# Kernel optimization log

Hardware: AMD Instinct MI355X
Metric: run time of the kernel (lower is better)

The kernel has to match this reference:

```python
import jax, jax.numpy as jnp
import numpy as np

COMMITMENT_COST = 0.25
EPS = 1e-10


def setup_inputs() -> dict:
    key = jax.random.key(0)
    k1, k2 = jax.random.split(key)
    B, C, H, W = 16, 64, 128, 128          # C == embedding_dim
    K, D = 512, 64                          # codebook size, embedding_dim
    inputs = jax.random.normal(k1, (B, C, H, W), dtype=jnp.float32)
    # nn.Embedding init: uniform(-1/K, 1/K)
    embedding = jax.random.uniform(k2, (K, D), dtype=jnp.float32,
                                   minval=-1.0 / K, maxval=1.0 / K)
    return {"inputs": inputs, "embedding": embedding}


def reference(inputs, embedding):
    # NCHW -> NHWC, flatten to tokens [N, D]
    x = jnp.transpose(inputs, (0, 2, 3, 1))
    nhwc_shape = x.shape
    flat = x.reshape(-1, embedding.shape[1])                       # [N, D]

    distances = (jnp.sum(flat * flat, axis=1, keepdims=True)
                 + jnp.sum(embedding * embedding, axis=1)
                 - 2.0 * flat @ embedding.T)
    idx = jnp.argmin(distances, axis=1)                            # [N]

    # one-hot encodings (returned), quantized via direct gather
    encodings = jax.nn.one_hot(idx, embedding.shape[0], dtype=flat.dtype)  # [N, K]
    quantized = embedding[idx].reshape(nhwc_shape)                 # [B,H,W,D]

    e_latent = jnp.mean((jax.lax.stop_gradient(quantized) - x) ** 2)
    q_latent = jnp.mean((quantized - jax.lax.stop_gradient(x)) ** 2)
    loss = q_latent + COMMITMENT_COST * e_latent

    # straight-through estimator
    quantized_st = x + jax.lax.stop_gradient(quantized - x)

    avg_probs = jnp.mean(encodings, axis=0)                        # [K]
    perplexity = jnp.exp(-jnp.sum(avg_probs * jnp.log(avg_probs + EPS)))

    return (loss, jnp.transpose(quantized_st, (0, 3, 1, 2)), perplexity, encodings)
```

## Files before the change

### kernel.cpp

```cpp
#include <hip/hip_runtime.h>
#include <math.h>


#define NTOK    262144
#define KCODES  512
#define DDIM    64
#define CSTRIDE 16384
#define IMG     1048576
#define QOFF    1
#define POFF    16777217
#define EOFF    16777218
#define BK      8192
#define LOSS    8704
#define EBF     12800
#define SUBFLT  32768

typedef short bf16x8 __attribute__((ext_vector_type(8)));
typedef float f32x4  __attribute__((ext_vector_type(4)));

__device__ __forceinline__ unsigned short f2bf(float f) {
    unsigned u = __float_as_uint(f);
    return (unsigned short)((u + 0x7fffu + ((u >> 16) & 1u)) >> 16);
}

__device__ __forceinline__ float np_pairwise_sq64(const float* v) {
    float r[8];
#pragma unroll
    for (int j = 0; j < 8; ++j) r[j] = __fmul_rn(v[j], v[j]);
#pragma unroll
    for (int i = 8; i < 64; i += 8) {
#pragma unroll
        for (int j = 0; j < 8; ++j)
            r[j] = __fadd_rn(r[j], __fmul_rn(v[i + j], v[i + j]));
    }
    float s01 = __fadd_rn(r[0], r[1]);
    float s23 = __fadd_rn(r[2], r[3]);
    float s45 = __fadd_rn(r[4], r[5]);
    float s67 = __fadd_rn(r[6], r[7]);
    return __fadd_rn(__fadd_rn(s01, s23), __fadd_rn(s45, s67));
}

__global__ __launch_bounds__(256) void vq_prep(const float* __restrict__ emb,
                                               float* __restrict__ out,
                                               float* __restrict__ ws) {
    const int tid = threadIdx.x, blk = blockIdx.x;
    if (blk >= 9) {
        f32x4* sub4 = (f32x4*)(out + EOFF) + (size_t)(blk - 9) * 8192;
        const f32x4 z4 = {0.f, 0.f, 0.f, 0.f};
#pragma unroll
        for (int ii = 0; ii < 32; ++ii)
            sub4[ii * 256 + tid] = z4;
        return;
    }
    if (blk < 8) {
        unsigned short* ebf = (unsigned short*)(ws + EBF);
#pragma unroll
        for (int ii = 0; ii < 16; ++ii) {
            int t = blk * 4096 + ii * 256 + tid;
            ebf[t] = f2bf(emb[t]);
        }
    } else {
#pragma unroll
        for (int r = 0; r < 2; ++r) {
            const int k = tid * 2 + r;
            const float* e = emb + (size_t)k * DDIM;
            float v[64];
#pragma unroll
            for (int i = 0; i < 64; ++i) v[i] = e[i];
            ws[BK + k] = np_pairwise_sq64(v);
        }
    }
}

__global__ __launch_bounds__(256, 4) void vq_main(const float* __restrict__ in,
                                                  const float* __restrict__ emb,
                                                  float* __restrict__ out,
                                                  float* __restrict__ ws) {
    __shared__ unsigned short xbf[64 * 68];
    __shared__ float          xls[64 * 64];
    __shared__ float          bsh[512];
    __shared__ int            idx_sh[64];
    __shared__ float          red[4];

    const int tid = threadIdx.x, blk = blockIdx.x;
    const int T0 = blk * 64, b = T0 >> 14, hw0 = T0 & 16383;

    const float4* gx = (const float4*)(in + (size_t)b * IMG + hw0);
    float4 g[4];
#pragma unroll
    for (int jj = 0; jj < 4; ++jj) {
        int t = tid + jj * 256;
        g[jj] = gx[(size_t)(t >> 4) * (CSTRIDE / 4) + (t & 15)];
    }
    const float bk0 = ws[BK + tid];
    const float bk1 = ws[BK + 256 + tid];

#pragma unroll
    for (int jj = 0; jj < 4; ++jj) {
        int t = tid + jj * 256;
        int c = t >> 4, q4 = (t & 15) * 4;
        *(float4*)(&xls[c * 64 + q4]) = g[jj];
        xbf[(q4 + 0) * 68 + c] = f2bf(g[jj].x);
        xbf[(q4 + 1) * 68 + c] = f2bf(g[jj].y);
        xbf[(q4 + 2) * 68 + c] = f2bf(g[jj].z);
        xbf[(q4 + 3) * 68 + c] = f2bf(g[jj].w);
    }
    bsh[tid]       = bk0;
    bsh[256 + tid] = bk1;
    __syncthreads();

    const int l = tid & 63, w = tid >> 6;
    const int lm = l & 15, lg = l >> 4;

    const bf16x8 a0 = *(const bf16x8*)(xbf + (w * 16 + lm) * 68 + lg * 8);
    const bf16x8 a1 = *(const bf16x8*)(xbf + (w * 16 + lm) * 68 + 32 + lg * 8);

    const unsigned short* ebf = (const unsigned short*)(ws + EBF);
    const unsigned short* ep  = ebf + lm * 64 + lg * 8;

    float dmin[4]; int idx[4];
#pragma unroll
    for (int r = 0; r < 4; ++r) { dmin[r] = 3.402823466e38f; idx[r] = 0; }
    const f32x4 zero = {0.f, 0.f, 0.f, 0.f};

#pragma unroll 4
    for (int nt = 0; nt < 32; ++nt) {
        bf16x8 b0 = *(const bf16x8*)(ep + nt * 1024);
        bf16x8 b1 = *(const bf16x8*)(ep + nt * 1024 + 32);
        f32x4 acc = __builtin_amdgcn_mfma_f32_16x16x32_bf16(a0, b0, zero, 0, 0, 0);
        acc       = __builtin_amdgcn_mfma_f32_16x16x32_bf16(a1, b1, acc,  0, 0, 0);
        const int   code = nt * 16 + lm;
        const float bk   = bsh[code];
#pragma unroll
        for (int r = 0; r < 4; ++r) {
            float s = fmaf(-2.0f, acc[r], bk);
            if (s < dmin[r]) { dmin[r] = s; idx[r] = code; }
        }
    }

#pragma unroll
    for (int m = 1; m < 16; m <<= 1) {
#pragma unroll
        for (int r = 0; r < 4; ++r) {
            float od = __shfl_xor(dmin[r], m, 64);
            int   oi = __shfl_xor(idx[r],  m, 64);
            if (od < dmin[r] || (od == dmin[r] && oi < idx[r])) {
                dmin[r] = od; idx[r] = oi;
            }
        }
    }
    if (lm == 0) {
#pragma unroll
        for (int r = 0; r < 4; ++r) idx_sh[w * 16 + lg * 4 + r] = idx[r];
    }
    __syncthreads();

    const int tl = tid & 63, chh = (tid >> 6) * 16;
    const int id = idx_sh[tl];

    const float4* e4 = (const float4*)(emb + (size_t)id * DDIM + chh);
    float4 ev[4];
#pragma unroll
    for (int k = 0; k < 4; ++k) ev[k] = e4[k];

    float* q = out + QOFF + (size_t)b * IMG + hw0 + tl;
    float lsum = 0.f;
#pragma unroll
    for (int cc = 0; cc < 16; ++cc) {
        float x   = xls[(chh + cc) * 64 + tl];
        float ee  = ((const float*)&ev[cc >> 2])[cc & 3];
        float dqx = __fsub_rn(ee, x);
        lsum = __fadd_rn(lsum, __fmul_rn(dqx, dqx));
        __builtin_nontemporal_store(__fadd_rn(x, dqx),
                                    q + (size_t)(chh + cc) * CSTRIDE);
    }
#pragma unroll
    for (int off = 32; off > 0; off >>= 1) lsum += __shfl_down(lsum, off, 64);
    if ((tid & 63) == 0) red[tid >> 6] = lsum;
    __syncthreads();
    if (tid == 0) ws[LOSS + blk] = red[0] + red[1] + red[2] + red[3];

    if (tid < 64) {
        const int ix = idx_sh[tid];
        __builtin_nontemporal_store(
            1.0f, out + EOFF + (size_t)blk * SUBFLT + tid * 512 + ix);
        atomicAdd((int*)ws + ((blk & 15) << 9) + ix, 1);
    }
}

__global__ void vq_final(float* __restrict__ out, const float* __restrict__ ws) {
    __shared__ float sl[512], sp[512];
    int t = threadIdx.x;
    float s = 0.f;
#pragma unroll
    for (int r = 0; r < 8; ++r) s += ws[LOSS + t + 512 * r];
    sl[t] = s;
    int cnt = 0;
#pragma unroll
    for (int r = 0; r < 16; ++r) cnt += ((const int*)ws)[(r << 9) + t];
    float p = (float)cnt * (1.0f / 262144.0f);
    sp[t] = p * logf(p + 1e-10f);
    __syncthreads();
    for (int off = 256; off > 0; off >>= 1) {
        if (t < off) { sl[t] += sl[t + off]; sp[t] += sp[t + off]; }
        __syncthreads();
    }
    if (t == 0) {
        float m = sl[0] * (1.0f / 16777216.0f);
        out[0]    = __fadd_rn(m, __fmul_rn(0.25f, m));
        out[POFF] = expf(-sp[0]);
    }
}

extern "C" void kernel_launch(void* const* d_in, const int* in_sizes, int n_in,
                              void* d_out, int out_size, void* d_ws, size_t ws_size,
                              hipStream_t stream) {
    const float* in  = (const float*)d_in[0];
    const float* emb = (const float*)d_in[1];
    float* out = (float*)d_out;
    float* ws  = (float*)d_ws;

    (void)hipMemsetAsync(d_ws, 0, 16 * 512 * sizeof(int), stream);
    hipLaunchKernelGGL(vq_prep,  dim3(4105), dim3(256), 0, stream, emb, out, ws);
    hipLaunchKernelGGL(vq_main,  dim3(4096), dim3(256), 0, stream, in, emb, out, ws);
    hipLaunchKernelGGL(vq_final, dim3(1),    dim3(512), 0, stream, out, ws);
}
```

Baseline: 740.1 us.

## Move one-hot zeroing into main kernel and split quantized write into separate pass

The zero-fill of the one-hot encodings moves from the prep kernel into vq_main, so each block clears its own 64x512 slice with nontemporal vector stores, and the slice base is offset by two floats to keep the vector stores aligned. The quantized/loss write is taken out of vq_main into a new vq_qwrite kernel. It reads the input again together with a uint16 index array stored in workspace, and gathers embedding values per channel in a coalesced pattern. This drops the big xls shared buffer from vq_main, which may help occupancy. In exchange the 64 MB input is read a second time and one more kernel launch is added.

After: 754.4 us. About the same (+1.9%).

```diff
diff --git a/kernel.cpp b/kernel.cpp
--- a/kernel.cpp
+++ b/kernel.cpp
@@ -13,10 +13,12 @@
 #define BK      8192
 #define LOSS    8704
 #define EBF     12800
+#define IDXOFF  29184
 #define SUBFLT  32768
 
 typedef short bf16x8 __attribute__((ext_vector_type(8)));
 typedef float f32x4  __attribute__((ext_vector_type(4)));
+typedef float f32x2  __attribute__((ext_vector_type(2)));
 
 __device__ __forceinline__ unsigned short f2bf(float f) {
     unsigned u = __float_as_uint(f);
@@ -41,17 +43,8 @@
 }
 
 __global__ __launch_bounds__(256) void vq_prep(const float* __restrict__ emb,
-                                               float* __restrict__ out,
                                                float* __restrict__ ws) {
     const int tid = threadIdx.x, blk = blockIdx.x;
-    if (blk >= 9) {
-        f32x4* sub4 = (f32x4*)(out + EOFF) + (size_t)(blk - 9) * 8192;
-        const f32x4 z4 = {0.f, 0.f, 0.f, 0.f};
-#pragma unroll
-        for (int ii = 0; ii < 32; ++ii)
-            sub4[ii * 256 + tid] = z4;
-        return;
-    }
     if (blk < 8) {
         unsigned short* ebf = (unsigned short*)(ws + EBF);
 #pragma unroll
@@ -77,10 +70,8 @@
                                                   float* __restrict__ out,
                                                   float* __restrict__ ws) {
     __shared__ unsigned short xbf[64 * 68];
-    __shared__ float          xls[64 * 64];
     __shared__ float          bsh[512];
     __shared__ int            idx_sh[64];
-    __shared__ float          red[4];
 
     const int tid = threadIdx.x, blk = blockIdx.x;
     const int T0 = blk * 64, b = T0 >> 14, hw0 = T0 & 16383;
@@ -95,11 +86,24 @@
     const float bk0 = ws[BK + tid];
     const float bk1 = ws[BK + 256 + tid];
 
+    {
+        float* sub0 = out + EOFF + (size_t)blk * SUBFLT;
+        const f32x4 z4 = {0.f, 0.f, 0.f, 0.f};
+        const f32x2 z2 = {0.f, 0.f};
+        f32x4* base4 = (f32x4*)(sub0 + 2);
+#pragma unroll
+        for (int ii = 0; ii < 32; ++ii) {
+            int c = ii * 256 + tid;
+            if (c < 8191) __builtin_nontemporal_store(z4, base4 + c);
+        }
+        if (tid == 0) __builtin_nontemporal_store(z2, (f32x2*)sub0);
+        if (tid == 1) __builtin_nontemporal_store(z2, (f32x2*)(sub0 + 32766));
+    }
+
 #pragma unroll
     for (int jj = 0; jj < 4; ++jj) {
         int t = tid + jj * 256;
         int c = t >> 4, q4 = (t & 15) * 4;
-        *(float4*)(&xls[c * 64 + q4]) = g[jj];
         xbf[(q4 + 0) * 68 + c] = f2bf(g[jj].x);
         xbf[(q4 + 1) * 68 + c] = f2bf(g[jj].y);
         xbf[(q4 + 2) * 68 + c] = f2bf(g[jj].z);
@@ -155,37 +159,45 @@
     }
     __syncthreads();
 
-    const int tl = tid & 63, chh = (tid >> 6) * 16;
-    const int id = idx_sh[tl];
-
-    const float4* e4 = (const float4*)(emb + (size_t)id * DDIM + chh);
-    float4 ev[4];
-#pragma unroll
-    for (int k = 0; k < 4; ++k) ev[k] = e4[k];
-
-    float* q = out + QOFF + (size_t)b * IMG + hw0 + tl;
+    if (tid < 64) {
+        const int ix = idx_sh[tid];
+        ((unsigned short*)(ws + IDXOFF))[T0 + tid] = (unsigned short)ix;
+        __builtin_nontemporal_store(
+            1.0f, out + EOFF + ((size_t)T0 + tid) * 512 + ix);
+        atomicAdd((int*)ws + ((blk & 15) << 9) + ix, 1);
+    }
+}
+
+__global__ __launch_bounds__(256) void vq_qwrite(const float* __restrict__ in,
+                                                 const float* __restrict__ emb,
+                                                 float* __restrict__ out,
+                                                 float* __restrict__ ws) {
+    __shared__ float red[4];
+    const int tid = threadIdx.x, blk = blockIdx.x;
+    const int b = blk >> 8, c = (blk >> 2) & 63, qd = blk & 3;
+
+    const size_t base = (size_t)b * IMG + (size_t)c * CSTRIDE + qd * 4096;
+    const float*          px   = in + base;
+    float*                pq   = out + QOFF + base;
+    const unsigned short* pidx = (const unsigned short*)(ws + IDXOFF)
+                                 + b * CSTRIDE + qd * 4096;
+
     float lsum = 0.f;
 #pragma unroll
-    for (int cc = 0; cc < 16; ++cc) {
-        float x   = xls[(chh + cc) * 64 + tl];
-        float ee  = ((const float*)&ev[cc >> 2])[cc & 3];
-        float dqx = __fsub_rn(ee, x);
-        lsum = __fadd_rn(lsum, __fmul_rn(dqx, dqx));
-        __builtin_nontemporal_store(__fadd_rn(x, dqx),
-                                    q + (size_t)(chh + cc) * CSTRIDE);
+    for (int i = 0; i < 16; ++i) {
+        const int j = i * 256 + tid;
+        float x = px[j];
+        int   k = pidx[j];
+        float e = emb[k * DDIM + c];
+        float d = __fsub_rn(e, x);
+        lsum = __fadd_rn(lsum, __fmul_rn(d, d));
+        pq[j] = __fadd_rn(x, d);
     }
 #pragma unroll
     for (int off = 32; off > 0; off >>= 1) lsum += __shfl_down(lsum, off, 64);
     if ((tid & 63) == 0) red[tid >> 6] = lsum;
     __syncthreads();
     if (tid == 0) ws[LOSS + blk] = red[0] + red[1] + red[2] + red[3];
-
-    if (tid < 64) {
-        const int ix = idx_sh[tid];
-        __builtin_nontemporal_store(
-            1.0f, out + EOFF + (size_t)blk * SUBFLT + tid * 512 + ix);
-        atomicAdd((int*)ws + ((blk & 15) << 9) + ix, 1);
-    }
 }
 
 __global__ void vq_final(float* __restrict__ out, const float* __restrict__ ws) {
@@ -221,7 +233,8 @@
     float* ws  = (float*)d_ws;
 
     (void)hipMemsetAsync(d_ws, 0, 16 * 512 * sizeof(int), stream);
-    hipLaunchKernelGGL(vq_prep,  dim3(4105), dim3(256), 0, stream, emb, out, ws);
-    hipLaunchKernelGGL(vq_main,  dim3(4096), dim3(256), 0, stream, in, emb, out, ws);
-    hipLaunchKernelGGL(vq_final, dim3(1),    dim3(512), 0, stream, out, ws);
-}
+    hipLaunchKernelGGL(vq_prep,   dim3(9),    dim3(256), 0, stream, emb, ws);
+    hipLaunchKernelGGL(vq_main,   dim3(4096), dim3(256), 0, stream, in, emb, out, ws);
+    hipLaunchKernelGGL(vq_qwrite, dim3(4096), dim3(256), 0, stream, in, emb, out, ws);
+    hipLaunchKernelGGL(vq_final,  dim3(1),    dim3(512), 0, stream, out, ws);
+}
```
